# Kernel optimization log

Hardware: AMD Instinct MI355X
Metric: run time of the kernel (lower is better)

Reference implementation:

```python
import jax, jax.numpy as jnp
import numpy as np

CHUNK = 16

def setup_inputs() -> dict:
    key = jax.random.key(0)
    k1, k2, k3, k4 = jax.random.split(key, 4)
    B, T, D, N = 2, 2048, 1024, 16
    u_input = jax.random.normal(k1, (B, T, D), dtype=jnp.float32)
    delta = jax.random.uniform(k2, (B, T, D), dtype=jnp.float32)
    b_mat = jax.random.normal(k3, (B, T, D, N), dtype=jnp.float32)
    c_mat = jax.random.normal(k4, (B, T, D, N), dtype=jnp.float32)
    A_log = jnp.log(jnp.linspace(1.0, float(N), N)).astype(jnp.float32)
    return {"u_input": u_input, "delta": delta, "b_mat": b_mat, "c_mat": c_mat, "A_log": A_log}

def reference(u_input, delta, b_mat, c_mat, A_log):
    B, T, D = u_input.shape
    N = A_log.shape[0]
    L = min(CHUNK, T)
    C = T // L  # T chosen divisible by chunk size
    A = -jnp.exp(A_log)  # [N], broadcasts over [B,L,D,N]

    # reshape into chunks and move chunk axis first for lax.scan
    u_c = jnp.moveaxis(u_input.reshape(B, C, L, D), 1, 0)       # [C,B,L,D]
    d_c = jnp.moveaxis(delta.reshape(B, C, L, D), 1, 0)        # [C,B,L,D]
    b_c = jnp.moveaxis(b_mat.reshape(B, C, L, D, N), 1, 0)     # [C,B,L,D,N]
    c_c = jnp.moveaxis(c_mat.reshape(B, C, L, D, N), 1, 0)     # [C,B,L,D,N]

    def step(h, inp):
        u, dl, b, c = inp  # u,dl: [B,L,D]; b,c: [B,L,D,N]; h: [B,D,N]
        deltaA = jnp.clip(dl[..., None] * A, -10.0, 10.0)      # [B,L,D,N]
        eA = jnp.exp(deltaA)
        frac = jnp.where(jnp.abs(deltaA) < 1e-4,
                         dl[..., None],
                         (eA - 1.0) / (A + 1e-12))
        Bu = frac * (b * u[..., None])                          # [B,L,D,N]
        Ah_cum = jnp.cumprod(eA, axis=1)
        h_expand = h[:, None] * Ah_cum                          # [B,L,D,N]
        # flip_weights[t] = eA[t] for t < L-1, and 1 at t = L-1
        fw = jnp.concatenate([eA[:, :-1], jnp.ones_like(eA[:, :1])], axis=1)
        Bu_term = jnp.flip(jnp.cumsum(Bu * fw, axis=1), axis=1)
        h_new = h_expand + Bu_term
        y = (h_new * c).sum(-1)                                 # [B,L,D]
        return h_new[:, -1], y

    h0 = jnp.zeros((B, D, N), dtype=u_input.dtype)
    _, ys = jax.lax.scan(step, h0, (u_c, d_c, b_c, c_c))        # ys: [C,B,L,D]
    return jnp.moveaxis(ys, 0, 1).reshape(B, T, D)
```

## Files before the change

kernel.cpp:

```cpp
#include <hip/hip_runtime.h>

#define BB 2
#define TT 2048
#define DD 1024
#define NN 16
#define LL 16
#define CC (TT / LL)

__global__ __launch_bounds__(256) void k1_carry(
    const float* __restrict__ delta,
    const float* __restrict__ u,
    const float* __restrict__ bmat,
    const float* __restrict__ A_log,
    float* __restrict__ hin,
    int S, int CPS)
{
    int g = blockIdx.x * 256 + threadIdx.x;
    int n = g & (NN - 1);
    int d = (g >> 4) & (DD - 1);
    int b = g >> 14;

    float A_n  = -__expf(A_log[n]);
    float rinv = 1.0f / (A_n + 1e-12f);

    float h = 0.0f;
    for (int c = 0; c < CC; ++c) {
        if ((c & (CPS - 1)) == 0) {
            int seg = c / CPS;
            hin[((b * S + seg) * DD + d) * NN + n] = h;
        }
        int t0 = c * LL;
        int base = (b * TT + t0) * DD + d;

        float dl[LL];
        #pragma unroll
        for (int t = 0; t < LL; ++t) dl[t] = delta[base + t * DD];
        float bm0 = bmat[base * NN + n];
        float uu0 = u[base];

        float p = 1.0f;
        float Q = 0.0f;
        #pragma unroll
        for (int t = 0; t < LL; ++t) {
            float dA = fminf(fmaxf(dl[t] * A_n, -10.0f), 10.0f);
            float eA = __expf(dA);
            if (t == 0) {
                float frac = (fabsf(dA) < 1e-4f) ? dl[t] : (eA - 1.0f) * rinv;
                Q = frac * (bm0 * uu0) * eA;
            }
            p *= eA;
        }
        h = h * p + Q;
    }
}

__global__ __launch_bounds__(256) void k2_main(
    const float* __restrict__ delta,
    const float* __restrict__ u,
    const float* __restrict__ bmat,
    const float* __restrict__ cmat,
    const float* __restrict__ A_log,
    const float* __restrict__ hin,
    float* __restrict__ out,
    int S, int CPS)
{
    const int dblks = DD / 16;
    int blocks_per_b = S * dblks;
    int b   = blockIdx.x / blocks_per_b;
    int r   = blockIdx.x - b * blocks_per_b;
    int seg = r / dblks;
    int dblk = r - seg * dblks;

    int n = threadIdx.x & 15;
    int d = dblk * 16 + (threadIdx.x >> 4);

    float A_n  = -__expf(A_log[n]);
    float rinv = 1.0f / (A_n + 1e-12f);

    float h = hin[((b * S + seg) * DD + d) * NN + n];
    int t0seg = seg * (TT / S);

    for (int c = 0; c < CPS; ++c) {
        int t0 = t0seg + c * LL;
        int base = (b * TT + t0) * DD + d;

        float dl[LL], bu[LL], cm[LL];
        #pragma unroll
        for (int t = 0; t < LL; ++t) {
            int bt = base + t * DD;
            dl[t] = delta[bt];
            float uu = u[bt];
            float bm = bmat[bt * NN + n];
            cm[t] = cmat[bt * NN + n];
            bu[t] = bm * uu;
        }

        float cp[LL], pref[LL];
        float prun = 1.0f, srun = 0.0f;
        #pragma unroll
        for (int t = 0; t < LL; ++t) {
            float dA = fminf(fmaxf(dl[t] * A_n, -10.0f), 10.0f);
            float eA = __expf(dA);
            float frac = (fabsf(dA) < 1e-4f) ? dl[t] : (eA - 1.0f) * rinv;
            float Bu = frac * bu[t];
            float gg = Bu * ((t < LL - 1) ? eA : 1.0f);
            prun *= eA;
            cp[t] = prun;
            srun += gg;
            pref[t] = srun;
        }

        float yv = 0.0f;
        #pragma unroll
        for (int t = 0; t < LL; ++t) {
            float hn = h * cp[t] + pref[LL - 1 - t];
            float v  = hn * cm[t];
            v += __shfl_xor(v, 1);
            v += __shfl_xor(v, 2);
            v += __shfl_xor(v, 4);
            v += __shfl_xor(v, 8);
            if (n == t) yv = v;
        }
        h = h * cp[LL - 1] + pref[0];

        out[base + n * DD] = yv;
    }
}

extern "C" void kernel_launch(void* const* d_in, const int* in_sizes, int n_in,
                              void* d_out, int out_size, void* d_ws, size_t ws_size,
                              hipStream_t stream) {
    (void)in_sizes; (void)n_in; (void)out_size;

    const float* u     = (const float*)d_in[0];
    const float* delta = (const float*)d_in[1];
    const float* bmat  = (const float*)d_in[2];
    const float* cmat  = (const float*)d_in[3];
    const float* A_log = (const float*)d_in[4];
    float* out = (float*)d_out;
    float* hin = (float*)d_ws;

    int S = 32;
    while ((size_t)BB * (size_t)S * DD * NN * sizeof(float) > ws_size && S > 1)
        S >>= 1;
    int CPS = CC / S;

    k1_carry<<<BB * DD * NN / 256, 256, 0, stream>>>(delta, u, bmat, A_log, hin, S, CPS);
    k2_main<<<BB * S * (DD / 16), 256, 0, stream>>>(delta, u, bmat, cmat, A_log, hin, out, S, CPS);
}
```

Baseline: 681.3 us.

## Split serial carry pass into parallel segment transforms plus short scan

The carry kernel that walked all chunks serially per (b,d,n) becomes two kernels. One computes each segment's affine transform (P,Q) in parallel across 32 segments. The other does a short 32-step scan to produce the segment-start states. This removes the long serial dependency chain and the low parallelism of the old carry kernel, at the cost of an extra launch and writing and reading the P/Q tables. The workspace-size check was dropped, so it now assumes the workspace holds three tables.

```diff
diff --git a/kernel.cpp b/kernel.cpp
--- a/kernel.cpp
+++ b/kernel.cpp
@@ -7,28 +7,27 @@
 #define LL 16
 #define CC (TT / LL)
 
-__global__ __launch_bounds__(256) void k1_carry(
+__global__ __launch_bounds__(256) void k1a_segxform(
     const float* __restrict__ delta,
     const float* __restrict__ u,
     const float* __restrict__ bmat,
     const float* __restrict__ A_log,
-    float* __restrict__ hin,
+    float* __restrict__ Pseg,
+    float* __restrict__ Qseg,
     int S, int CPS)
 {
     int g = blockIdx.x * 256 + threadIdx.x;
-    int n = g & (NN - 1);
-    int d = (g >> 4) & (DD - 1);
-    int b = g >> 14;
+    int n   = g & (NN - 1);
+    int d   = (g >> 4) & (DD - 1);
+    int seg = (g >> 14) & (S - 1);
+    int b   = g >> (14 + 5);
 
     float A_n  = -__expf(A_log[n]);
     float rinv = 1.0f / (A_n + 1e-12f);
 
-    float h = 0.0f;
-    for (int c = 0; c < CC; ++c) {
-        if ((c & (CPS - 1)) == 0) {
-            int seg = c / CPS;
-            hin[((b * S + seg) * DD + d) * NN + n] = h;
-        }
+    float P = 1.0f, Q = 0.0f;
+    int c0 = seg * CPS;
+    for (int c = c0; c < c0 + CPS; ++c) {
         int t0 = c * LL;
         int base = (b * TT + t0) * DD + d;
 
@@ -39,18 +38,39 @@
         float uu0 = u[base];
 
         float p = 1.0f;
-        float Q = 0.0f;
+        float q = 0.0f;
         #pragma unroll
         for (int t = 0; t < LL; ++t) {
             float dA = fminf(fmaxf(dl[t] * A_n, -10.0f), 10.0f);
             float eA = __expf(dA);
             if (t == 0) {
                 float frac = (fabsf(dA) < 1e-4f) ? dl[t] : (eA - 1.0f) * rinv;
-                Q = frac * (bm0 * uu0) * eA;
+                q = frac * (bm0 * uu0) * eA;
             }
             p *= eA;
         }
-        h = h * p + Q;
+        P = P * p;
+        Q = Q * p + q;
+    }
+    Pseg[g] = P;
+    Qseg[g] = Q;
+}
+
+__global__ __launch_bounds__(256) void k1b_scan(
+    const float* __restrict__ Pseg,
+    const float* __restrict__ Qseg,
+    float* __restrict__ hin,
+    int S)
+{
+    int g = blockIdx.x * 256 + threadIdx.x;
+    int dn = g & (DD * NN - 1);
+    int b  = g >> 14;
+
+    float h = 0.0f;
+    for (int s = 0; s < S; ++s) {
+        int idx = (b * S + s) * (DD * NN) + dn;
+        hin[idx] = h;
+        h = h * Pseg[idx] + Qseg[idx];
     }
 }
 
@@ -138,13 +158,19 @@
     const float* cmat  = (const float*)d_in[3];
     const float* A_log = (const float*)d_in[4];
     float* out = (float*)d_out;
-    float* hin = (float*)d_ws;
 
-    int S = 32;
-    while ((size_t)BB * (size_t)S * DD * NN * sizeof(float) > ws_size && S > 1)
-        S >>= 1;
-    int CPS = CC / S;
+    const int S = 32;
+    const int CPS = CC / S;
 
-    k1_carry<<<BB * DD * NN / 256, 256, 0, stream>>>(delta, u, bmat, A_log, hin, S, CPS);
-    k2_main<<<BB * S * (DD / 16), 256, 0, stream>>>(delta, u, bmat, cmat, A_log, hin, out, S, CPS);
+    size_t tbl = (size_t)BB * S * DD * NN;
+    float* Pseg = (float*)d_ws;
+    float* Qseg = Pseg + tbl;
+    float* hin  = Qseg + tbl;
+    (void)ws_size;
+
+    k1a_segxform<<<(BB * S * DD * NN) / 256, 256, 0, stream>>>(
+        delta, u, bmat, A_log, Pseg, Qseg, S, CPS);
+    k1b_scan<<<(BB * DD * NN) / 256, 256, 0, stream>>>(Pseg, Qseg, hin, S);
+    k2_main<<<BB * S * (DD / 16), 256, 0, stream>>>(
+        delta, u, bmat, cmat, A_log, hin, out, S, CPS);
 }
```

Measured after the change: 597.6 us. 12.3% less time.
